# Kernel tuning notes

Measured on AMD Instinct MI355X. Metric: run time of the kernel, lower is better.

The kernel has to match this reference:

```python
import jax, jax.numpy as jnp
import numpy as np

B, T, DIN, H, NOUT = 256, 512, 64, 512, 128


def setup_inputs() -> dict:
    key = jax.random.key(0)
    ks = jax.random.split(key, 11)
    s = 1.0 / np.sqrt(H)  # PyTorch GRU init scale
    inp = {"x": jax.random.normal(ks[0], (B, T, DIN), dtype=jnp.float32)}
    # layer 0 (input DIN), layer 1 (input H); gate order: r, z, n
    inp["w_ih0"] = jax.random.uniform(ks[1], (3 * H, DIN), minval=-s, maxval=s)
    inp["w_hh0"] = jax.random.uniform(ks[2], (3 * H, H), minval=-s, maxval=s)
    inp["b_ih0"] = jax.random.uniform(ks[3], (3 * H,), minval=-s, maxval=s)
    inp["b_hh0"] = jax.random.uniform(ks[4], (3 * H,), minval=-s, maxval=s)
    inp["w_ih1"] = jax.random.uniform(ks[5], (3 * H, H), minval=-s, maxval=s)
    inp["w_hh1"] = jax.random.uniform(ks[6], (3 * H, H), minval=-s, maxval=s)
    inp["b_ih1"] = jax.random.uniform(ks[7], (3 * H,), minval=-s, maxval=s)
    inp["b_hh1"] = jax.random.uniform(ks[8], (3 * H,), minval=-s, maxval=s)
    inp["w_fc"] = jax.random.uniform(ks[9], (NOUT, H), minval=-s, maxval=s)
    inp["b_fc"] = jax.random.uniform(ks[10], (NOUT,), minval=-s, maxval=s)
    return inp


def _gru_layer(x_seq, w_ih, w_hh, b_ih, b_hh):
    # x_seq: [B, T, Din] -> hidden trajectory [B, T, H]
    xg = jnp.einsum('btd,gd->btg', x_seq, w_ih) + b_ih  # [B, T, 3H], precomputed input gates
    h0 = jnp.zeros((x_seq.shape[0], w_hh.shape[1]), dtype=x_seq.dtype)

    def step(h, xg_t):
        hg = h @ w_hh.T + b_hh
        xr, xz, xn = jnp.split(xg_t, 3, axis=-1)
        hr, hz, hn = jnp.split(hg, 3, axis=-1)
        r = jax.nn.sigmoid(xr + hr)
        z = jax.nn.sigmoid(xz + hz)
        n = jnp.tanh(xn + r * hn)
        h_new = (1.0 - z) * n + z * h
        return h_new, h_new

    _, hs = jax.lax.scan(step, h0, jnp.swapaxes(xg, 0, 1))  # [T, B, H]
    return jnp.swapaxes(hs, 0, 1)


def reference(x, w_ih0, w_hh0, b_ih0, b_hh0, w_ih1, w_hh1, b_ih1, b_hh1, w_fc, b_fc):
    h1 = _gru_layer(x, w_ih0, w_hh0, b_ih0, b_hh0)   # [B, T, H]
    h2 = _gru_layer(h1, w_ih1, w_hh1, b_ih1, b_hh1)  # [B, T, H]
    last = h2[:, -1, :]                               # [B, H]
    return last @ w_fc.T + b_fc                       # [B, NOUT]
```

## Files before the change

kernel.cpp:

```cpp
#include <hip/hip_runtime.h>
#include <math.h>

typedef unsigned short u16;
typedef __attribute__((ext_vector_type(8))) short s8v;
typedef __attribute__((ext_vector_type(4))) float f4v;
typedef __attribute__((ext_vector_type(4))) int   i4v;

constexpr int kB    = 256;
constexpr int kT    = 512;
constexpr int kDIN  = 64;
constexpr int kH    = 512;
constexpr int kG3   = 1536;
constexpr int kNOUT = 128;
constexpr int kPlane = 8 * 2 * 16 * 512;
constexpr int kXStep = 16 * 2 * 512;

#define MFMA16 __builtin_amdgcn_mfma_f32_16x16x32_bf16

__device__ __forceinline__ u16 f2bf(float f) {
  union { float f; unsigned u; } v; v.f = f;
  unsigned r = (v.u + 0x7FFFu + ((v.u >> 16) & 1u)) >> 16;
  return (u16)r;
}
__device__ __forceinline__ float fsig(float x) {
  x = fminf(fmaxf(x, -30.f), 30.f);
  float e = __expf(-x);
  return __fdividef(1.f, 1.f + e);
}
__device__ __forceinline__ float ftanh(float x) {
  x = fminf(fmaxf(x, -15.f), 15.f);
  float e = __expf(-2.f * x);
  return __fdividef(1.f - e, 1.f + e);
}

__device__ __forceinline__ void load16_nw(const u16* base, i4v a[16]) {
  asm volatile(
      "global_load_dwordx4 %0, %16, off sc0 sc1\n\t"
      "global_load_dwordx4 %1, %16, off offset:1024 sc0 sc1\n\t"
      "global_load_dwordx4 %2, %16, off offset:2048 sc0 sc1\n\t"
      "global_load_dwordx4 %3, %16, off offset:3072 sc0 sc1\n\t"
      "global_load_dwordx4 %4, %17, off sc0 sc1\n\t"
      "global_load_dwordx4 %5, %17, off offset:1024 sc0 sc1\n\t"
      "global_load_dwordx4 %6, %17, off offset:2048 sc0 sc1\n\t"
      "global_load_dwordx4 %7, %17, off offset:3072 sc0 sc1\n\t"
      "global_load_dwordx4 %8, %18, off sc0 sc1\n\t"
      "global_load_dwordx4 %9, %18, off offset:1024 sc0 sc1\n\t"
      "global_load_dwordx4 %10, %18, off offset:2048 sc0 sc1\n\t"
      "global_load_dwordx4 %11, %18, off offset:3072 sc0 sc1\n\t"
      "global_load_dwordx4 %12, %19, off sc0 sc1\n\t"
      "global_load_dwordx4 %13, %19, off offset:1024 sc0 sc1\n\t"
      "global_load_dwordx4 %14, %19, off offset:2048 sc0 sc1\n\t"
      "global_load_dwordx4 %15, %19, off offset:3072 sc0 sc1"
      : "=&v"(a[0]), "=&v"(a[1]), "=&v"(a[2]), "=&v"(a[3]),
        "=&v"(a[4]), "=&v"(a[5]), "=&v"(a[6]), "=&v"(a[7]),
        "=&v"(a[8]), "=&v"(a[9]), "=&v"(a[10]), "=&v"(a[11]),
        "=&v"(a[12]), "=&v"(a[13]), "=&v"(a[14]), "=&v"(a[15])
      : "v"(base), "v"(base + 4 * 512), "v"(base + 8 * 512), "v"(base + 12 * 512)
      : "memory");
}

__device__ __forceinline__ void store_h_l0(
    u16* p0, u16* p1, u16* p2, u16* p3,
    u16* q0, u16* q1, u16* q2, u16* q3,
    unsigned v0, unsigned v1, unsigned v2, unsigned v3) {
  asm volatile(
      "global_store_short %0, %8, off sc0 sc1\n\t"
      "global_store_short %1, %9, off sc0 sc1\n\t"
      "global_store_short %2, %10, off sc0 sc1\n\t"
      "global_store_short %3, %11, off sc0 sc1\n\t"
      "global_store_short %4, %8, off\n\t"
      "global_store_short %5, %9, off\n\t"
      "global_store_short %6, %10, off\n\t"
      "global_store_short %7, %11, off\n\t"
      "s_waitcnt vmcnt(4)"
      :: "v"(p0), "v"(p1), "v"(p2), "v"(p3),
         "v"(q0), "v"(q1), "v"(q2), "v"(q3),
         "v"(v0), "v"(v1), "v"(v2), "v"(v3)
      : "memory");
}
__device__ __forceinline__ void store_h_l1(
    u16* p0, u16* p1, u16* p2, u16* p3,
    unsigned v0, unsigned v1, unsigned v2, unsigned v3) {
  asm volatile(
      "global_store_short %0, %4, off sc0 sc1\n\t"
      "global_store_short %1, %5, off sc0 sc1\n\t"
      "global_store_short %2, %6, off sc0 sc1\n\t"
      "global_store_short %3, %7, off sc0 sc1\n\t"
      "s_waitcnt vmcnt(0)"
      :: "v"(p0), "v"(p1), "v"(p2), "v"(p3),
         "v"(v0), "v"(v1), "v"(v2), "v"(v3)
      : "memory");
}

__global__ void build_wslab(const float* __restrict__ w, u16* __restrict__ d) {
  int idx  = blockIdx.x * 256 + threadIdx.x;
  int lane = idx & 63, fg = idx >> 6;
  int jt = fg / 96, f = fg % 96;
  int nt = f >> 4, kt = f & 15;
  int g = nt >> 1, u = nt & 1;
  int row = g * 512 + jt * 32 + u * 16 + (lane & 15);
  int k0  = kt * 32 + (lane >> 4) * 8;
  const float* src = w + (size_t)row * 512 + k0;
  u16* dst = d + ((size_t)fg) * 512 + lane * 8;
#pragma unroll
  for (int i = 0; i < 8; i++) dst[i] = f2bf(src[i]);
}

__global__ void build_wslab_ih0(const float* __restrict__ w, u16* __restrict__ d) {
  int idx  = blockIdx.x * 256 + threadIdx.x;
  int lane = idx & 63, fg = idx >> 6;
  int jt = fg / 12, f = fg % 12;
  int nt = f >> 1, kt = f & 1;
  int g = nt >> 1, u = nt & 1;
  int row = g * 512 + jt * 32 + u * 16 + (lane & 15);
  int k0  = kt * 32 + (lane >> 4) * 8;
  const float* src = w + (size_t)row * kDIN + k0;
  u16* dst = d + ((size_t)fg) * 512 + lane * 8;
#pragma unroll
  for (int i = 0; i < 8; i++) dst[i] = f2bf(src[i]);
}

__global__ void build_xplane(const float* __restrict__ x, u16* __restrict__ d) {
  int idx  = blockIdx.x * 256 + threadIdx.x;
  int lane = idx & 63, fg = idx >> 6;
  int kt = fg & 1, m = (fg >> 1) & 15, T = fg >> 5;
  int b  = m * 16 + (lane & 15);
  int k0 = kt * 32 + (lane >> 4) * 8;
  const float* src = x + ((size_t)b * kT + T) * kDIN + k0;
  u16* dst = d + ((size_t)fg) * 512 + lane * 8;
#pragma unroll
  for (int i = 0; i < 8; i++) dst[i] = f2bf(src[i]);
}

__global__ __launch_bounds__(256, 1)
void rec_fused(int c, int TC, int nc, unsigned bar_base16, unsigned* bar,
               const u16* __restrict__ xpl,
               const u16* __restrict__ slab0hh, const u16* __restrict__ slab0ih,
               const u16* __restrict__ slab1hh, const u16* __restrict__ slab1ih,
               const float* __restrict__ bih0, const float* __restrict__ bhh0,
               const float* __restrict__ bih1, const float* __restrict__ bhh1,
               u16* __restrict__ h1pl, u16* __restrict__ hbuf,
               float* __restrict__ carry) {
  __shared__ u16 ldsw[96 * 512];

  const int bid   = blockIdx.x;
  const int layer = bid >> 7;
  const int lb    = bid & 127;
  const int jt    = lb & 15, bt = lb >> 4;
  const int cc    = (layer == 0) ? c : c - 1;
  const bool active = (cc >= 0 && cc < nc);

  unsigned* mybar = bar + (size_t)(layer * 8 + bt) * 64;

  if (!active) {
    if (threadIdx.x == 0)
      __hip_atomic_fetch_add(mybar, (unsigned)TC, __ATOMIC_RELAXED,
                             __HIP_MEMORY_SCOPE_AGENT);
    return;
  }

  const int tid   = threadIdx.x;
  const int wv    = tid >> 6, lane = tid & 63;
  const int mt    = wv >> 1, u = wv & 1;
  const int jl    = lane & 15;
  const int jg    = jt * 32 + u * 16 + jl;
  const int mrow  = (lane >> 4) * 4;
  const int bbase = bt * 32 + mt * 16 + mrow;

  const size_t cons_off = ((size_t)((bt * 2 + mt) * 16)) * 512 + lane * 8;
  const size_t prod_off = ((size_t)((bt * 2 + mt) * 16 + jt)) * 512 +
                          (size_t)(16 * (u * 2 + (jl >> 3))) * 8 + (jl & 7);
  float* mycarry = carry + (size_t)layer * kB * kH;

  if (layer == 0) {
    s8v bh[3][16];
    {
      const u16* base = slab0hh + (size_t)jt * 96 * 512 + (size_t)lane * 8;
#pragma unroll
      for (int g = 0; g < 3; ++g)
#pragma unroll
        for (int kt = 0; kt < 16; ++kt)
          bh[g][kt] = *(const s8v*)(base + (size_t)((g * 2 + u) * 16 + kt) * 512);
    }
    s8v bx[3][2];
    {
      const u16* base = slab0ih + (size_t)jt * 12 * 512 + (size_t)lane * 8;
#pragma unroll
      for (int g = 0; g < 3; ++g)
#pragma unroll
        for (int kt = 0; kt < 2; ++kt)
          bx[g][kt] = *(const s8v*)(base + (size_t)((g * 2 + u) * 2 + kt) * 512);
    }
    const float br  = bih0[jg] + bhh0[jg];
    const float bz  = bih0[512 + jg] + bhh0[512 + jg];
    const float bni = bih0[1024 + jg], bnh = bhh0[1024 + jg];

    float hp[4];
#pragma unroll
    for (int r = 0; r < 4; ++r)
      hp[r] = mycarry[(size_t)(bbase + r) * 512 + jg];

    const size_t xoff = (size_t)((bt * 2 + mt) * 2) * 512 + (size_t)lane * 8;
    const u16* xb0 = xpl + (size_t)(cc * TC) * kXStep + xoff;
    s8v ax0 = *(const s8v*)xb0;
    s8v ax1 = *(const s8v*)(xb0 + 512);

    for (int t = 0; t < TC; ++t) {
      if (tid == 0) {
        unsigned tgt = bar_base16 + 16u * (unsigned)t;
        int guard = 0;
        while (__hip_atomic_load(mybar, __ATOMIC_RELAXED,
                                 __HIP_MEMORY_SCOPE_AGENT) < tgt
               && ++guard < (1 << 21))
          __builtin_amdgcn_s_sleep(1);
      }
      __syncthreads();

      i4v a[16];
      load16_nw(hbuf + (size_t)(t & 1) * kPlane + cons_off, a);

      const f4v z4 = {0.f, 0.f, 0.f, 0.f};
      f4v acc0, acc1, acc2, acc2x;
      acc0  = MFMA16(ax0, bx[0][0], z4, 0, 0, 0);
      acc0  = MFMA16(ax1, bx[0][1], acc0, 0, 0, 0);
      acc1  = MFMA16(ax0, bx[1][0], z4, 0, 0, 0);
      acc1  = MFMA16(ax1, bx[1][1], acc1, 0, 0, 0);
      acc2x = MFMA16(ax0, bx[2][0], z4, 0, 0, 0);
      acc2x = MFMA16(ax1, bx[2][1], acc2x, 0, 0, 0);
      acc2  = z4;
      asm volatile("s_waitcnt vmcnt(0)" ::: "memory");
      __builtin_amdgcn_sched_barrier(0);
#pragma unroll
      for (int kt = 0; kt < 16; ++kt) {
        const s8v av = __builtin_bit_cast(s8v, a[kt]);
        acc0 = MFMA16(av, bh[0][kt], acc0, 0, 0, 0);
        acc1 = MFMA16(av, bh[1][kt], acc1, 0, 0, 0);
        acc2 = MFMA16(av, bh[2][kt], acc2, 0, 0, 0);
      }

      unsigned hv[4];
#pragma unroll
      for (int r = 0; r < 4; ++r) {
        float rr = fsig(acc0[r] + br);
        float zz = fsig(acc1[r] + bz);
        float nn = ftanh(acc2x[r] + bni + rr * (acc2[r] + bnh));
        float hn = (1.f - zz) * nn + zz * hp[r];
        hp[r] = hn;
        hv[r] = f2bf(hn);
      }

      u16* pb = hbuf + (size_t)((t + 1) & 1) * kPlane + prod_off;
      u16* qb = h1pl + (size_t)((cc & 1) * TC + t) * kPlane + prod_off;
      store_h_l0(pb + (size_t)(mrow + 0) * 8, pb + (size_t)(mrow + 1) * 8,
                 pb + (size_t)(mrow + 2) * 8, pb + (size_t)(mrow + 3) * 8,
                 qb + (size_t)(mrow + 0) * 8, qb + (size_t)(mrow + 1) * 8,
                 qb + (size_t)(mrow + 2) * 8, qb + (size_t)(mrow + 3) * 8,
                 hv[0], hv[1], hv[2], hv[3]);
      __syncthreads();
      if (tid == 0)
        __hip_atomic_fetch_add(mybar, 1u, __ATOMIC_RELAXED,
                               __HIP_MEMORY_SCOPE_AGENT);
      if (t + 1 < TC) {
        const u16* xb = xpl + (size_t)(cc * TC + t + 1) * kXStep + xoff;
        ax0 = *(const s8v*)xb;
        ax1 = *(const s8v*)(xb + 512);
      }
    }
#pragma unroll
    for (int r = 0; r < 4; ++r)
      mycarry[(size_t)(bbase + r) * 512 + jg] = hp[r];
  } else {
    {
      const u16* src = slab1ih + (size_t)jt * 96 * 512;
      for (int i = tid; i < 96 * 512 / 8; i += 256)
        *(s8v*)&ldsw[i * 8] = *(const s8v*)&src[i * 8];
    }
    s8v bh[3][16];
    {
      const u16* base = slab1hh + (size_t)jt * 96 * 512 + (size_t)lane * 8;
#pragma unroll
      for (int g = 0; g < 3; ++g)
#pragma unroll
        for (int kt = 0; kt < 16; ++kt)
          bh[g][kt] = *(const s8v*)(base + (size_t)((g * 2 + u) * 16 + kt) * 512);
    }
    const float br  = bih1[jg] + bhh1[jg];
    const float bz  = bih1[512 + jg] + bhh1[512 + jg];
    const float bni = bih1[1024 + jg], bnh = bhh1[1024 + jg];

    float hp[4];
#pragma unroll
    for (int r = 0; r < 4; ++r)
      hp[r] = mycarry[(size_t)(bbase + r) * 512 + jg];

    const u16* h1base = h1pl + (size_t)((cc & 1) * TC) * kPlane + cons_off;
    s8v a1[16];
#pragma unroll
    for (int kt = 0; kt < 16; ++kt)
      a1[kt] = *(const s8v*)(h1base + (size_t)kt * 512);

    for (int t = 0; t < TC; ++t) {
      if (tid == 0) {
        unsigned tgt = bar_base16 + 16u * (unsigned)t;
        int guard = 0;
        while (__hip_atomic_load(mybar, __ATOMIC_RELAXED,
                                 __HIP_MEMORY_SCOPE_AGENT) < tgt
               && ++guard < (1 << 21))
          __builtin_amdgcn_s_sleep(1);
      }
      __syncthreads();

      i4v a2[16];
      load16_nw(hbuf + (size_t)(2 + (t & 1)) * kPlane + cons_off, a2);

      const f4v z4 = {0.f, 0.f, 0.f, 0.f};
      f4v acc0 = z4, acc1 = z4, acc2 = z4, acc2x = z4;
#pragma unroll
      for (int kt = 0; kt < 16; ++kt) {
        const s8v b0 = *(const s8v*)&ldsw[(size_t)((0 + u) * 16 + kt) * 512 + lane * 8];
        const s8v b1 = *(const s8v*)&ldsw[(size_t)((2 + u) * 16 + kt) * 512 + lane * 8];
        const s8v b2 = *(const s8v*)&ldsw[(size_t)((4 + u) * 16 + kt) * 512 + lane * 8];
        acc0  = MFMA16(a1[kt], b0, acc0, 0, 0, 0);
        acc1  = MFMA16(a1[kt], b1, acc1, 0, 0, 0);
        acc2x = MFMA16(a1[kt], b2, acc2x, 0, 0, 0);
      }
      asm volatile("s_waitcnt vmcnt(0)" ::: "memory");
      __builtin_amdgcn_sched_barrier(0);
#pragma unroll
      for (int kt = 0; kt < 16; ++kt) {
        const s8v av = __builtin_bit_cast(s8v, a2[kt]);
        acc0 = MFMA16(av, bh[0][kt], acc0, 0, 0, 0);
        acc1 = MFMA16(av, bh[1][kt], acc1, 0, 0, 0);
        acc2 = MFMA16(av, bh[2][kt], acc2, 0, 0, 0);
      }

      unsigned hv[4];
#pragma unroll
      for (int r = 0; r < 4; ++r) {
        float rr = fsig(acc0[r] + br);
        float zz = fsig(acc1[r] + bz);
        float nn = ftanh(acc2x[r] + bni + rr * (acc2[r] + bnh));
        float hn = (1.f - zz) * nn + zz * hp[r];
        hp[r] = hn;
        hv[r] = f2bf(hn);
      }

      u16* pb = hbuf + (size_t)(2 + ((t + 1) & 1)) * kPlane + prod_off;
      store_h_l1(pb + (size_t)(mrow + 0) * 8, pb + (size_t)(mrow + 1) * 8,
                 pb + (size_t)(mrow + 2) * 8, pb + (size_t)(mrow + 3) * 8,
                 hv[0], hv[1], hv[2], hv[3]);
      __syncthreads();
      if (tid == 0)
        __hip_atomic_fetch_add(mybar, 1u, __ATOMIC_RELAXED,
                               __HIP_MEMORY_SCOPE_AGENT);
      if (t + 1 < TC) {
        const u16* hb = h1base + (size_t)(t + 1) * kPlane;
#pragma unroll
        for (int kt = 0; kt < 16; ++kt)
          a1[kt] = *(const s8v*)(hb + (size_t)kt * 512);
      }
    }
#pragma unroll
    for (int r = 0; r < 4; ++r)
      mycarry[(size_t)(bbase + r) * 512 + jg] = hp[r];
  }
}

__global__ __launch_bounds__(128)
void fc_kernel(const float* __restrict__ h, const float* __restrict__ wfc,
               const float* __restrict__ bfc, float* __restrict__ out) {
  const int b = blockIdx.x;
  const int n = threadIdx.x;
  const float* hrow = h + (size_t)b * kH;
  const float* wrow = wfc + (size_t)n * kH;
  float acc = 0.f;
#pragma unroll 4
  for (int k = 0; k < kH; k += 4) {
    const float4 hv = *(const float4*)&hrow[k];
    const float4 wv = *(const float4*)&wrow[k];
    acc = fmaf(hv.x, wv.x, acc); acc = fmaf(hv.y, wv.y, acc);
    acc = fmaf(hv.z, wv.z, acc); acc = fmaf(hv.w, wv.w, acc);
  }
  out[(size_t)b * kNOUT + n] = acc + bfc[n];
}

extern "C" void kernel_launch(void* const* d_in, const int* in_sizes, int n_in,
                              void* d_out, int out_size, void* d_ws, size_t ws_size,
                              hipStream_t stream) {
  const float* x     = (const float*)d_in[0];
  const float* w_ih0 = (const float*)d_in[1];
  const float* w_hh0 = (const float*)d_in[2];
  const float* b_ih0 = (const float*)d_in[3];
  const float* b_hh0 = (const float*)d_in[4];
  const float* w_ih1 = (const float*)d_in[5];
  const float* w_hh1 = (const float*)d_in[6];
  const float* b_ih1 = (const float*)d_in[7];
  const float* b_hh1 = (const float*)d_in[8];
  const float* w_fc  = (const float*)d_in[9];
  const float* b_fc  = (const float*)d_in[10];
  float* out = (float*)d_out;

  auto need = [](int tc) -> size_t {
    size_t s = 0;
    s += 3 * (size_t)kG3 * kH * 2;
    s += (size_t)kG3 * kDIN * 2;
    s += (size_t)kT * kXStep * 2;
    s += 2 * (size_t)tc * kPlane * 2;
    s += 4 * (size_t)kPlane * 2;
    s += 2 * (size_t)kB * kH * 4;
    s += 65536;
    return s;
  };
  int TC = 64;
  while (TC > 2 && need(TC) > ws_size) TC >>= 1;
  const int nc = kT / TC;

  char* p = (char*)d_ws;
  auto carve = [&](size_t bytes) {
    char* r = p; p += (bytes + 255) & ~(size_t)255; return r;
  };
  u16* slab0hh = (u16*)carve((size_t)kG3 * kH * 2);
  u16* slab1hh = (u16*)carve((size_t)kG3 * kH * 2);
  u16* slab1ih = (u16*)carve((size_t)kG3 * kH * 2);
  u16* slab0ih = (u16*)carve((size_t)kG3 * kDIN * 2);
  u16* xpl     = (u16*)carve((size_t)kT * kXStep * 2);
  u16* h1pl    = (u16*)carve(2 * (size_t)TC * kPlane * 2);
  u16* hbuf    = (u16*)carve(4 * (size_t)kPlane * 2);
  float* carry = (float*)carve(2 * (size_t)kB * kH * 4);
  unsigned* bar = (unsigned*)carve(32 * 64 * sizeof(unsigned));

  build_wslab<<<384, 256, 0, stream>>>(w_hh0, slab0hh);
  build_wslab<<<384, 256, 0, stream>>>(w_hh1, slab1hh);
  build_wslab<<<384, 256, 0, stream>>>(w_ih1, slab1ih);
  build_wslab_ih0<<<48, 256, 0, stream>>>(w_ih0, slab0ih);
  build_xplane<<<4096, 256, 0, stream>>>(x, xpl);
  hipMemsetAsync(hbuf, 0, 4 * (size_t)kPlane * 2 + 2 * (size_t)kB * kH * 4, stream);
  hipMemsetAsync(bar, 0, 32 * 64 * sizeof(unsigned), stream);

  for (int c = 0; c <= nc; ++c) {
    unsigned base16 = (unsigned)c * 16u * (unsigned)TC;
    rec_fused<<<dim3(256), dim3(256), 0, stream>>>(
        c, TC, nc, base16, bar, xpl,
        slab0hh, slab0ih, slab1hh, slab1ih,
        b_ih0, b_hh0, b_ih1, b_hh1,
        h1pl, hbuf, carry);
  }

  fc_kernel<<<dim3(kB), dim3(kNOUT), 0, stream>>>(
      carry + (size_t)kB * kH, w_fc, b_fc, out);
}
```

Before: 2.327 ms.

## Replace block-level barrier with per-wave sub-counters for finer-grained recurrence sync

Replaces the per-block spin-wait plus __syncthreads and single-counter arrive with per-wave counters. Each wave waits only on the two producer sub-counters for its own M-tile and increments its own counter after storing h. This removes two block-wide barriers per timestep and lets waves in a block run out of lockstep. The risk is memory-ordering correctness, because stores and relaxed atomics have no release fence between them. It also doubles the barrier storage and multiplies polling traffic.

New measurement: 2.863 ms. 23.0% more time.

```diff
diff --git a/kernel.cpp b/kernel.cpp
--- a/kernel.cpp
+++ b/kernel.cpp
@@ -147,21 +147,26 @@
   const int layer = bid >> 7;
   const int lb    = bid & 127;
   const int jt    = lb & 15, bt = lb >> 4;
+  const int gid   = layer * 8 + bt;
   const int cc    = (layer == 0) ? c : c - 1;
   const bool active = (cc >= 0 && cc < nc);
-
-  unsigned* mybar = bar + (size_t)(layer * 8 + bt) * 64;
-
-  if (!active) {
-    if (threadIdx.x == 0)
-      __hip_atomic_fetch_add(mybar, (unsigned)TC, __ATOMIC_RELAXED,
-                             __HIP_MEMORY_SCOPE_AGENT);
-    return;
-  }
 
   const int tid   = threadIdx.x;
   const int wv    = tid >> 6, lane = tid & 63;
   const int mt    = wv >> 1, u = wv & 1;
+
+  unsigned* subbase = bar + (size_t)(gid * 4) * 64;
+  unsigned* mysub   = subbase + (size_t)wv * 64;
+  unsigned* w0sub   = subbase + (size_t)(mt * 2 + 0) * 64;
+  unsigned* w1sub   = subbase + (size_t)(mt * 2 + 1) * 64;
+
+  if (!active) {
+    if (tid < 4)
+      __hip_atomic_fetch_add(subbase + (size_t)tid * 64, (unsigned)TC,
+                             __ATOMIC_RELAXED, __HIP_MEMORY_SCOPE_AGENT);
+    return;
+  }
+
   const int jl    = lane & 15;
   const int jg    = jt * 32 + u * 16 + jl;
   const int mrow  = (lane >> 4) * 4;
@@ -172,6 +177,23 @@
                           (size_t)(16 * (u * 2 + (jl >> 3))) * 8 + (jl & 7);
   float* mycarry = carry + (size_t)layer * kB * kH;
 
+  auto wave_wait = [&](unsigned tgt) {
+    if ((tid & 63) == 0) {
+      int guard = 0;
+      while ((__hip_atomic_load(w0sub, __ATOMIC_RELAXED,
+                                __HIP_MEMORY_SCOPE_AGENT) < tgt ||
+              __hip_atomic_load(w1sub, __ATOMIC_RELAXED,
+                                __HIP_MEMORY_SCOPE_AGENT) < tgt) &&
+             ++guard < (1 << 21))
+        __builtin_amdgcn_s_sleep(1);
+    }
+  };
+  auto wave_arrive = [&]() {
+    if ((tid & 63) == 0)
+      __hip_atomic_fetch_add(mysub, 1u, __ATOMIC_RELAXED,
+                             __HIP_MEMORY_SCOPE_AGENT);
+  };
+
   if (layer == 0) {
     s8v bh[3][16];
     {
@@ -206,15 +228,7 @@
     s8v ax1 = *(const s8v*)(xb0 + 512);
 
     for (int t = 0; t < TC; ++t) {
-      if (tid == 0) {
-        unsigned tgt = bar_base16 + 16u * (unsigned)t;
-        int guard = 0;
-        while (__hip_atomic_load(mybar, __ATOMIC_RELAXED,
-                                 __HIP_MEMORY_SCOPE_AGENT) < tgt
-               && ++guard < (1 << 21))
-          __builtin_amdgcn_s_sleep(1);
-      }
-      __syncthreads();
+      if (t) wave_wait(bar_base16 + 16u * (unsigned)t);
 
       i4v a[16];
       load16_nw(hbuf + (size_t)(t & 1) * kPlane + cons_off, a);
@@ -228,6 +242,7 @@
       acc2x = MFMA16(ax0, bx[2][0], z4, 0, 0, 0);
       acc2x = MFMA16(ax1, bx[2][1], acc2x, 0, 0, 0);
       acc2  = z4;
+      __builtin_amdgcn_sched_barrier(0);
       asm volatile("s_waitcnt vmcnt(0)" ::: "memory");
       __builtin_amdgcn_sched_barrier(0);
 #pragma unroll
@@ -256,10 +271,7 @@
                  qb + (size_t)(mrow + 0) * 8, qb + (size_t)(mrow + 1) * 8,
                  qb + (size_t)(mrow + 2) * 8, qb + (size_t)(mrow + 3) * 8,
                  hv[0], hv[1], hv[2], hv[3]);
-      __syncthreads();
-      if (tid == 0)
-        __hip_atomic_fetch_add(mybar, 1u, __ATOMIC_RELAXED,
-                               __HIP_MEMORY_SCOPE_AGENT);
+      wave_arrive();
       if (t + 1 < TC) {
         const u16* xb = xpl + (size_t)(cc * TC + t + 1) * kXStep + xoff;
         ax0 = *(const s8v*)xb;
@@ -275,6 +287,7 @@
       for (int i = tid; i < 96 * 512 / 8; i += 256)
         *(s8v*)&ldsw[i * 8] = *(const s8v*)&src[i * 8];
     }
+    __syncthreads();
     s8v bh[3][16];
     {
       const u16* base = slab1hh + (size_t)jt * 96 * 512 + (size_t)lane * 8;
@@ -300,15 +313,7 @@
       a1[kt] = *(const s8v*)(h1base + (size_t)kt * 512);
 
     for (int t = 0; t < TC; ++t) {
-      if (tid == 0) {
-        unsigned tgt = bar_base16 + 16u * (unsigned)t;
-        int guard = 0;
-        while (__hip_atomic_load(mybar, __ATOMIC_RELAXED,
-                                 __HIP_MEMORY_SCOPE_AGENT) < tgt
-               && ++guard < (1 << 21))
-          __builtin_amdgcn_s_sleep(1);
-      }
-      __syncthreads();
+      if (t) wave_wait(bar_base16 + 16u * (unsigned)t);
 
       i4v a2[16];
       load16_nw(hbuf + (size_t)(2 + (t & 1)) * kPlane + cons_off, a2);
@@ -324,6 +329,7 @@
         acc1  = MFMA16(a1[kt], b1, acc1, 0, 0, 0);
         acc2x = MFMA16(a1[kt], b2, acc2x, 0, 0, 0);
       }
+      __builtin_amdgcn_sched_barrier(0);
       asm volatile("s_waitcnt vmcnt(0)" ::: "memory");
       __builtin_amdgcn_sched_barrier(0);
 #pragma unroll
@@ -349,10 +355,7 @@
       store_h_l1(pb + (size_t)(mrow + 0) * 8, pb + (size_t)(mrow + 1) * 8,
                  pb + (size_t)(mrow + 2) * 8, pb + (size_t)(mrow + 3) * 8,
                  hv[0], hv[1], hv[2], hv[3]);
-      __syncthreads();
-      if (tid == 0)
-        __hip_atomic_fetch_add(mybar, 1u, __ATOMIC_RELAXED,
-                               __HIP_MEMORY_SCOPE_AGENT);
+      wave_arrive();
       if (t + 1 < TC) {
         const u16* hb = h1base + (size_t)(t + 1) * kPlane;
 #pragma unroll
@@ -408,7 +411,7 @@
     s += 2 * (size_t)tc * kPlane * 2;
     s += 4 * (size_t)kPlane * 2;
     s += 2 * (size_t)kB * kH * 4;
-    s += 65536;
+    s += 131072;
     return s;
   };
   int TC = 64;
@@ -427,7 +430,7 @@
   u16* h1pl    = (u16*)carve(2 * (size_t)TC * kPlane * 2);
   u16* hbuf    = (u16*)carve(4 * (size_t)kPlane * 2);
   float* carry = (float*)carve(2 * (size_t)kB * kH * 4);
-  unsigned* bar = (unsigned*)carve(32 * 64 * sizeof(unsigned));
+  unsigned* bar = (unsigned*)carve(64 * 64 * sizeof(unsigned));
 
   build_wslab<<<384, 256, 0, stream>>>(w_hh0, slab0hh);
   build_wslab<<<384, 256, 0, stream>>>(w_hh1, slab1hh);
@@ -435,7 +438,7 @@
   build_wslab_ih0<<<48, 256, 0, stream>>>(w_ih0, slab0ih);
   build_xplane<<<4096, 256, 0, stream>>>(x, xpl);
   hipMemsetAsync(hbuf, 0, 4 * (size_t)kPlane * 2 + 2 * (size_t)kB * kH * 4, stream);
-  hipMemsetAsync(bar, 0, 32 * 64 * sizeof(unsigned), stream);
+  hipMemsetAsync(bar, 0, 64 * 64 * sizeof(unsigned), stream);
 
   for (int c = 0; c <= nc; ++c) {
     unsigned base16 = (unsigned)c * 16u * (unsigned)TC;
```
